# Kernel tuning notes

Hardware: AMD Instinct MI355X
Metric: run time of the kernel (lower is better)

## Reference

```python
import jax, jax.numpy as jnp
import numpy as np

B, K, D = 16384, 64, 256
H, HD = 2, 128  # n_heads, head_dim


def setup_inputs() -> dict:
    key = jax.random.key(0)
    ks = jax.random.split(key, 8)
    center_emb = jax.random.normal(ks[0], (B, D), dtype=jnp.float32)
    neighbor_emb = jax.random.normal(ks[1], (B, K, D), dtype=jnp.float32)
    neighbor_weights = jax.random.normal(ks[2], (B, K), dtype=jnp.float32)
    neighbor_mask = jax.random.randint(ks[3], (B, K), 0, 2).astype(bool)
    s = 1.0 / np.sqrt(D)
    Wq = jax.random.normal(ks[4], (H, HD, D), dtype=jnp.float32) * s   # per-head q proj
    Wk = jax.random.normal(ks[5], (H, HD, D), dtype=jnp.float32) * s   # per-head k proj
    Wout = jax.random.normal(ks[6], (D, H * D), dtype=jnp.float32) * (1.0 / np.sqrt(H * D))
    Wgate = jax.random.normal(ks[7], (D, 2 * D), dtype=jnp.float32) * (1.0 / np.sqrt(2 * D))
    return {"center_emb": center_emb, "neighbor_emb": neighbor_emb,
            "neighbor_weights": neighbor_weights, "neighbor_mask": neighbor_mask,
            "Wq": Wq, "Wk": Wk, "Wout": Wout, "Wgate": Wgate}


def reference(center_emb, neighbor_emb, neighbor_weights, neighbor_mask, Wq, Wk, Wout, Wgate):
    scale = 1.0 / jnp.sqrt(jnp.asarray(HD, dtype=center_emb.dtype))
    q = jnp.einsum('bd,hed->bhe', center_emb, Wq)          # [B,H,HD]
    k = jnp.einsum('bkd,hed->bhke', neighbor_emb, Wk)      # [B,H,K,HD]
    scores = jnp.einsum('bhe,bhke->bhk', q, k) * scale + neighbor_weights[:, None, :]
    scores = jnp.where(neighbor_mask[:, None, :], scores, jnp.asarray(-1e9, scores.dtype))
    attn = jax.nn.softmax(scores, axis=-1)                 # [B,H,K]
    ctx = jnp.einsum('bhk,bkd->bhd', attn, neighbor_emb)   # [B,H,D]
    multi_ctx = ctx.reshape(ctx.shape[0], H * D)           # concat heads along feature dim
    projected = multi_ctx @ Wout.T                         # [B,D]
    gate_in = jnp.concatenate([center_emb, projected], axis=-1)
    gate = jax.nn.sigmoid(gate_in @ Wgate.T)
    return gate * center_emb + (1.0 - gate) * projected
```

## Files before the change

kernel.cpp:

```cpp
#include <hip/hip_runtime.h>
#include <stdint.h>

typedef __attribute__((ext_vector_type(8))) short bf8;
typedef __attribute__((ext_vector_type(4))) float f4;

template<int CTRL>
__device__ __forceinline__ float dppMove(float v, float ident) {
  return __int_as_float(__builtin_amdgcn_update_dpp(
      __float_as_int(ident), __float_as_int(v), CTRL, 0xf, 0xf, false));
}
__device__ __forceinline__ float waveSum63(float v) {
  v += dppMove<0x128>(v, 0.f);
  v += dppMove<0x124>(v, 0.f);
  v += dppMove<0x122>(v, 0.f);
  v += dppMove<0x121>(v, 0.f);
  v += dppMove<0x142>(v, 0.f);
  v += dppMove<0x143>(v, 0.f);
  return v;
}
__device__ __forceinline__ float waveMax63(float v) {
  v = fmaxf(v, dppMove<0x128>(v, -3e38f));
  v = fmaxf(v, dppMove<0x124>(v, -3e38f));
  v = fmaxf(v, dppMove<0x122>(v, -3e38f));
  v = fmaxf(v, dppMove<0x121>(v, -3e38f));
  v = fmaxf(v, dppMove<0x142>(v, -3e38f));
  v = fmaxf(v, dppMove<0x143>(v, -3e38f));
  return v;
}
__device__ __forceinline__ float bcast63(float v) {
  return __int_as_float(__builtin_amdgcn_readlane(__float_as_int(v), 63));
}
__device__ __forceinline__ ushort f2bf(float f) {
  uint32_t b = __float_as_uint(f);
  uint32_t r = (b + 0x7fffu + ((b >> 16) & 1u)) >> 16;
  return (ushort)r;
}
__device__ __forceinline__ float bf2f(ushort u) {
  return __uint_as_float(((uint32_t)u) << 16);
}

__global__ __launch_bounds__(256)
void mhna_prologue(const float* __restrict__ center, ushort* __restrict__ centerBf,
                   const float* __restrict__ Wout, const float* __restrict__ Wgate,
                   ushort* __restrict__ Woutb, ushort* __restrict__ Wgb,
                   const float* __restrict__ Wq, const float* __restrict__ Wk,
                   ushort* __restrict__ Mtb) {
  const int blk = blockIdx.x;
  const int t = threadIdx.x;
  if (blk < 2048) {
    const int n4 = 16384 * 256 / 4;
    int i = blk * 256 + t;
    for (; i < n4; i += 2048 * 256) {
      float4 v = ((const float4*)center)[i];
      ushort4 u;
      u.x = f2bf(v.x); u.y = f2bf(v.y); u.z = f2bf(v.z); u.w = f2bf(v.w);
      ((ushort4*)centerBf)[i] = u;
    }
  } else if (blk < 2304) {
    const int n4 = 256 * 512 / 4;
    int i = (blk - 2048) * 256 + t;
    const float* s = (i < n4) ? Wout : Wgate;
    ushort* d = (i < n4) ? Woutb : Wgb;
    int j = (i < n4) ? i : i - n4;
    float4 v = ((const float4*)s)[j];
    ushort4 u;
    u.x = f2bf(v.x); u.y = f2bf(v.y); u.z = f2bf(v.z); u.w = f2bf(v.w);
    ((ushort4*)d)[j] = u;
  } else {
    const int n = blk - 2304;
    const int h = n >> 8, dk = n & 255;
    float acc = 0.f;
#pragma unroll 8
    for (int e = 0; e < 128; ++e) {
      float wkv = Wk[(size_t)(h * 128 + e) * 256 + dk];
      float wqv = Wq[(size_t)(h * 128 + e) * 256 + t];
      acc = fmaf(wqv, wkv, acc);
    }
    Mtb[(size_t)n * 256 + t] = f2bf(acc);
  }
}

__global__ __launch_bounds__(512)
void gemm_qM(const ushort* __restrict__ A, const ushort* __restrict__ W,
             ushort* __restrict__ Cb) {
  const int t = threadIdx.x;
  const int w = t >> 6, l = t & 63;
  const int row0 = blockIdx.x * 64;
  const int col0 = w * 64;
  const int lr = l & 15, lg = l >> 4;

  f4 acc[4][4];
#pragma unroll
  for (int i = 0; i < 4; ++i)
#pragma unroll
    for (int j = 0; j < 4; ++j) acc[i][j] = (f4)0.f;

#pragma unroll 2
  for (int kk = 0; kk < 256; kk += 32) {
    bf8 af[4];
#pragma unroll
    for (int i = 0; i < 4; ++i)
      af[i] = *(const bf8*)(A + (size_t)(row0 + i * 16 + lr) * 256 + kk + lg * 8);
#pragma unroll
    for (int j = 0; j < 4; ++j) {
      bf8 bw = *(const bf8*)(W + (size_t)(col0 + j * 16 + lr) * 256 + kk + lg * 8);
#pragma unroll
      for (int i = 0; i < 4; ++i)
        acc[i][j] = __builtin_amdgcn_mfma_f32_16x16x32_bf16(af[i], bw, acc[i][j], 0, 0, 0);
    }
  }
#pragma unroll
  for (int i = 0; i < 4; ++i)
#pragma unroll
    for (int j = 0; j < 4; ++j)
#pragma unroll
      for (int r = 0; r < 4; ++r)
        Cb[(size_t)(row0 + i * 16 + lg * 4 + r) * 512 + col0 + j * 16 + lr] =
            f2bf(acc[i][j][r]);
}

__global__ __launch_bounds__(256)
void mhna_kC(const float* __restrict__ nbg, const ushort* __restrict__ qMb,
             const float* __restrict__ wts, const int* __restrict__ msk,
             ushort* __restrict__ ctxb) {
  __shared__ float sc_s[2][64];
  __shared__ float at_s[2][64];
  __shared__ float part[4][512];
  const int b = blockIdx.x;
  const int t = threadIdx.x;
  const int w = t >> 6, lam = t & 63;

  const int mv_l = msk[(size_t)b * 64 + lam];
  const unsigned long long mb = __ballot(mv_l != 0);

  const ushort4* qm4 = (const ushort4*)(qMb + (size_t)b * 512);
  ushort4 ua = qm4[lam];
  ushort4 ub = qm4[64 + lam];
  f4 qa = {bf2f(ua.x), bf2f(ua.y), bf2f(ua.z), bf2f(ua.w)};
  f4 qb = {bf2f(ub.x), bf2f(ub.y), bf2f(ub.z), bf2f(ub.w)};

  const float4* nb4 = (const float4*)(nbg + (size_t)b * (64 * 256));
  float4 st[16];
#pragma unroll
  for (int r = 0; r < 16; ++r) {
    st[r] = make_float4(0.f, 0.f, 0.f, 0.f);
    const int k = r * 4 + w;
    if ((mb >> k) & 1ull) st[r] = nb4[k * 64 + lam];
  }

#pragma unroll
  for (int r = 0; r < 16; ++r) {
    const int k = r * 4 + w;
    if ((mb >> k) & 1ull) {
      float4 v = st[r];
      float p0 = v.x * qa.x + v.y * qa.y + v.z * qa.z + v.w * qa.w;
      float p1 = v.x * qb.x + v.y * qb.y + v.z * qb.z + v.w * qb.w;
      float s0 = waveSum63(p0);
      float s1 = waveSum63(p1);
      if (lam == 63) { sc_s[0][k] = s0; sc_s[1][k] = s1; }
    }
  }
  __syncthreads();

  if (t < 128) {
    const int h = w;
    float s = sc_s[h][lam];
    float wv = wts[(size_t)b * 64 + lam];
    s = mv_l ? fmaf(s, 0.08838834764831845f, wv) : -1e9f;
    float mx = bcast63(waveMax63(s));
    float e = __expf(s - mx);
    float sm = bcast63(waveSum63(e));
    at_s[h][lam] = e / sm;
  }
  __syncthreads();

  float c0[4] = {0.f, 0.f, 0.f, 0.f};
  float c1[4] = {0.f, 0.f, 0.f, 0.f};
#pragma unroll
  for (int r = 0; r < 16; ++r) {
    const int k = r * 4 + w;
    if ((mb >> k) & 1ull) {
      const float A0 = at_s[0][k];
      const float A1 = at_s[1][k];
      float4 v = st[r];
      c0[0] = fmaf(A0, v.x, c0[0]); c0[1] = fmaf(A0, v.y, c0[1]);
      c0[2] = fmaf(A0, v.z, c0[2]); c0[3] = fmaf(A0, v.w, c0[3]);
      c1[0] = fmaf(A1, v.x, c1[0]); c1[1] = fmaf(A1, v.y, c1[1]);
      c1[2] = fmaf(A1, v.z, c1[2]); c1[3] = fmaf(A1, v.w, c1[3]);
    }
  }
  f4 p0v = {c0[0], c0[1], c0[2], c0[3]};
  f4 p1v = {c1[0], c1[1], c1[2], c1[3]};
  *(f4*)&part[w][lam * 4]       = p0v;
  *(f4*)&part[w][256 + lam * 4] = p1v;
  __syncthreads();

  float r0 = part[0][t] + part[1][t] + part[2][t] + part[3][t];
  float r1 = part[0][256 + t] + part[1][256 + t] + part[2][256 + t] + part[3][256 + t];
  ctxb[(size_t)b * 512 + t] = f2bf(r0);
  ctxb[(size_t)b * 512 + 256 + t] = f2bf(r1);
}

#define LDP 260
__global__ __launch_bounds__(512)
void mhna_PG(const ushort* __restrict__ ctxb, const ushort* __restrict__ Woutb,
             const ushort* __restrict__ centerBf, const ushort* __restrict__ Wgb,
             const float* __restrict__ centerF, float* __restrict__ out) {
  __shared__ float p_s[64][LDP];
  const int t = threadIdx.x;
  const int w = t >> 6, l = t & 63;
  const int row0 = blockIdx.x * 64;
  const int col0 = w * 32;
  const int lr = l & 15, lg = l >> 4;

  f4 acc1[4][2];
#pragma unroll
  for (int i = 0; i < 4; ++i)
#pragma unroll
    for (int j = 0; j < 2; ++j) acc1[i][j] = (f4)0.f;

#pragma unroll 2
  for (int kk = 0; kk < 512; kk += 32) {
    bf8 af[4];
#pragma unroll
    for (int i = 0; i < 4; ++i)
      af[i] = *(const bf8*)(ctxb + (size_t)(row0 + i * 16 + lr) * 512 + kk + lg * 8);
#pragma unroll
    for (int j = 0; j < 2; ++j) {
      bf8 bw = *(const bf8*)(Woutb + (size_t)(col0 + j * 16 + lr) * 512 + kk + lg * 8);
#pragma unroll
      for (int i = 0; i < 4; ++i)
        acc1[i][j] = __builtin_amdgcn_mfma_f32_16x16x32_bf16(af[i], bw, acc1[i][j], 0, 0, 0);
    }
  }
#pragma unroll
  for (int i = 0; i < 4; ++i)
#pragma unroll
    for (int j = 0; j < 2; ++j)
#pragma unroll
      for (int r = 0; r < 4; ++r)
        p_s[i * 16 + lg * 4 + r][col0 + j * 16 + lr] = acc1[i][j][r];
  __syncthreads();

  f4 acc2[4][2];
#pragma unroll
  for (int i = 0; i < 4; ++i)
#pragma unroll
    for (int j = 0; j < 2; ++j) acc2[i][j] = (f4)0.f;

#pragma unroll 2
  for (int kk = 0; kk < 256; kk += 32) {
    bf8 af[4];
#pragma unroll
    for (int i = 0; i < 4; ++i)
      af[i] = *(const bf8*)(centerBf + (size_t)(row0 + i * 16 + lr) * 256 + kk + lg * 8);
#pragma unroll
    for (int j = 0; j < 2; ++j) {
      bf8 bw = *(const bf8*)(Wgb + (size_t)(col0 + j * 16 + lr) * 512 + kk + lg * 8);
#pragma unroll
      for (int i = 0; i < 4; ++i)
        acc2[i][j] = __builtin_amdgcn_mfma_f32_16x16x32_bf16(af[i], bw, acc2[i][j], 0, 0, 0);
    }
  }
#pragma unroll 2
  for (int kk = 0; kk < 256; kk += 32) {
    bf8 af[4];
#pragma unroll
    for (int i = 0; i < 4; ++i) {
      f4 x0 = *(const f4*)&p_s[i * 16 + lr][kk + lg * 8];
      f4 x1 = *(const f4*)&p_s[i * 16 + lr][kk + lg * 8 + 4];
      bf8 a;
      a[0] = (short)f2bf(x0.x); a[1] = (short)f2bf(x0.y);
      a[2] = (short)f2bf(x0.z); a[3] = (short)f2bf(x0.w);
      a[4] = (short)f2bf(x1.x); a[5] = (short)f2bf(x1.y);
      a[6] = (short)f2bf(x1.z); a[7] = (short)f2bf(x1.w);
      af[i] = a;
    }
#pragma unroll
    for (int j = 0; j < 2; ++j) {
      bf8 bw = *(const bf8*)(Wgb + (size_t)(col0 + j * 16 + lr) * 512 + 256 + kk + lg * 8);
#pragma unroll
      for (int i = 0; i < 4; ++i)
        acc2[i][j] = __builtin_amdgcn_mfma_f32_16x16x32_bf16(af[i], bw, acc2[i][j], 0, 0, 0);
    }
  }

#pragma unroll
  for (int i = 0; i < 4; ++i)
#pragma unroll
    for (int j = 0; j < 2; ++j)
#pragma unroll
      for (int r = 0; r < 4; ++r) {
        const int lrow = i * 16 + lg * 4 + r;
        const int row = row0 + lrow;
        const int col = col0 + j * 16 + lr;
        float g = 1.f / (1.f + __expf(-acc2[i][j][r]));
        float pv = p_s[lrow][col];
        float cv = centerF[(size_t)row * 256 + col];
        out[(size_t)row * 256 + col] = g * cv + (1.f - g) * pv;
      }
}

extern "C" void kernel_launch(void* const* d_in, const int* in_sizes, int n_in,
                              void* d_out, int out_size, void* d_ws, size_t ws_size,
                              hipStream_t stream) {
  const float* center = (const float*)d_in[0];
  const float* neigh  = (const float*)d_in[1];
  const float* nw     = (const float*)d_in[2];
  const int*   nm     = (const int*)d_in[3];
  const float* Wq     = (const float*)d_in[4];
  const float* Wk     = (const float*)d_in[5];
  const float* Wout   = (const float*)d_in[6];
  const float* Wgate  = (const float*)d_in[7];
  float* out = (float*)d_out;

  char* ws = (char*)d_ws;
  size_t off = 0;
  ushort* Mtb      = (ushort*)(ws + off); off += (size_t)512 * 256 * 2;
  ushort* centerBf = (ushort*)(ws + off); off += (size_t)16384 * 256 * 2;
  ushort* qMb      = (ushort*)(ws + off); off += (size_t)16384 * 512 * 2;
  ushort* ctxb     = (ushort*)(ws + off); off += (size_t)16384 * 512 * 2;
  ushort* Woutb    = (ushort*)(ws + off); off += (size_t)256 * 512 * 2;
  ushort* Wgb      = (ushort*)(ws + off); off += (size_t)256 * 512 * 2;

  mhna_prologue<<<2816, 256, 0, stream>>>(center, centerBf, Wout, Wgate,
                                          Woutb, Wgb, Wq, Wk, Mtb);
  gemm_qM<<<256, 512, 0, stream>>>(centerBf, Mtb, qMb);
  mhna_kC<<<16384, 256, 0, stream>>>(neigh, qMb, nw, nm, ctxb);
  mhna_PG<<<256, 512, 0, stream>>>(ctxb, Woutb, centerBf, Wgb, center, out);
}
```

Baseline: 198.8 us.

## Use MFMA for attention scores, stage neighbors as bf16 in LDS, halve GEMM tiles

The attention kernel now converts each neighbor row to bf16, computes both heads' scores with one MFMA per K-slice, and stores the bf16 rows in a swizzled LDS tile. The context sum then reads that tile per output column, which removes the cross-wave partial-sum buffer and the DPP reductions. The two GEMM kernels switch to 32-row tiles with twice as many blocks to raise occupancy. The final blend reads center from the bf16 copy instead of fp32, so accuracy drops slightly and the output now depends on bf16 center values.

Measured after the change: 295.0 us. 1.48x slower.

```diff
diff --git a/kernel.cpp b/kernel.cpp
--- a/kernel.cpp
+++ b/kernel.cpp
@@ -1,4 +1,5 @@
 #include <hip/hip_runtime.h>
+#include <hip/hip_bf16.h>
 #include <stdint.h>
 
 typedef __attribute__((ext_vector_type(8))) short bf8;
@@ -85,32 +86,32 @@
              ushort* __restrict__ Cb) {
   const int t = threadIdx.x;
   const int w = t >> 6, l = t & 63;
-  const int row0 = blockIdx.x * 64;
+  const int row0 = blockIdx.x * 32;
   const int col0 = w * 64;
   const int lr = l & 15, lg = l >> 4;
 
-  f4 acc[4][4];
-#pragma unroll
-  for (int i = 0; i < 4; ++i)
+  f4 acc[2][4];
+#pragma unroll
+  for (int i = 0; i < 2; ++i)
 #pragma unroll
     for (int j = 0; j < 4; ++j) acc[i][j] = (f4)0.f;
 
 #pragma unroll 2
   for (int kk = 0; kk < 256; kk += 32) {
-    bf8 af[4];
-#pragma unroll
-    for (int i = 0; i < 4; ++i)
+    bf8 af[2];
+#pragma unroll
+    for (int i = 0; i < 2; ++i)
       af[i] = *(const bf8*)(A + (size_t)(row0 + i * 16 + lr) * 256 + kk + lg * 8);
 #pragma unroll
     for (int j = 0; j < 4; ++j) {
       bf8 bw = *(const bf8*)(W + (size_t)(col0 + j * 16 + lr) * 256 + kk + lg * 8);
 #pragma unroll
-      for (int i = 0; i < 4; ++i)
+      for (int i = 0; i < 2; ++i)
         acc[i][j] = __builtin_amdgcn_mfma_f32_16x16x32_bf16(af[i], bw, acc[i][j], 0, 0, 0);
     }
   }
 #pragma unroll
-  for (int i = 0; i < 4; ++i)
+  for (int i = 0; i < 2; ++i)
 #pragma unroll
     for (int j = 0; j < 4; ++j)
 #pragma unroll
@@ -123,118 +124,125 @@
 void mhna_kC(const float* __restrict__ nbg, const ushort* __restrict__ qMb,
              const float* __restrict__ wts, const int* __restrict__ msk,
              ushort* __restrict__ ctxb) {
+  __shared__ ushort nb_s[64][256];
   __shared__ float sc_s[2][64];
   __shared__ float at_s[2][64];
-  __shared__ float part[4][512];
   const int b = blockIdx.x;
   const int t = threadIdx.x;
-  const int w = t >> 6, lam = t & 63;
-
-  const int mv_l = msk[(size_t)b * 64 + lam];
+  const int w = t >> 6, l = t & 63;
+  const int lr = l & 15, lg = l >> 4;
+  const int krow = w * 16 + lr;
+
+  const int mv_l = msk[(size_t)b * 64 + l];
   const unsigned long long mb = __ballot(mv_l != 0);
-
-  const ushort4* qm4 = (const ushort4*)(qMb + (size_t)b * 512);
-  ushort4 ua = qm4[lam];
-  ushort4 ub = qm4[64 + lam];
-  f4 qa = {bf2f(ua.x), bf2f(ua.y), bf2f(ua.z), bf2f(ua.w)};
-  f4 qb = {bf2f(ub.x), bf2f(ub.y), bf2f(ub.z), bf2f(ub.w)};
-
-  const float4* nb4 = (const float4*)(nbg + (size_t)b * (64 * 256));
-  float4 st[16];
-#pragma unroll
-  for (int r = 0; r < 16; ++r) {
-    st[r] = make_float4(0.f, 0.f, 0.f, 0.f);
-    const int k = r * 4 + w;
-    if ((mb >> k) & 1ull) st[r] = nb4[k * 64 + lam];
-  }
-
-#pragma unroll
-  for (int r = 0; r < 16; ++r) {
-    const int k = r * 4 + w;
-    if ((mb >> k) & 1ull) {
-      float4 v = st[r];
-      float p0 = v.x * qa.x + v.y * qa.y + v.z * qa.z + v.w * qa.w;
-      float p1 = v.x * qb.x + v.y * qb.y + v.z * qb.z + v.w * qb.w;
-      float s0 = waveSum63(p0);
-      float s1 = waveSum63(p1);
-      if (lam == 63) { sc_s[0][k] = s0; sc_s[1][k] = s1; }
-    }
+  const bool rowOn = (mb >> krow) & 1ull;
+
+  const float* nbrow = nbg + (size_t)b * 16384 + (size_t)krow * 256 + lg * 8;
+  float4 a0[8], a1[8];
+#pragma unroll
+  for (int s = 0; s < 8; ++s) {
+    if (rowOn) {
+      a0[s] = *(const float4*)(nbrow + s * 32);
+      a1[s] = *(const float4*)(nbrow + s * 32 + 4);
+    } else {
+      a0[s] = make_float4(0.f, 0.f, 0.f, 0.f);
+      a1[s] = make_float4(0.f, 0.f, 0.f, 0.f);
+    }
+  }
+  bf8 bwv[8];
+#pragma unroll
+  for (int s = 0; s < 8; ++s) {
+    if (lr < 2)
+      bwv[s] = *(const bf8*)(qMb + (size_t)b * 512 + lr * 256 + s * 32 + lg * 8);
+    else
+      bwv[s] = (bf8)0;
+  }
+
+  f4 acc = {0.f, 0.f, 0.f, 0.f};
+  const int swz = (krow & 7) << 4;
+  char* ldsrow = (char*)&nb_s[krow][0];
+#pragma unroll
+  for (int s = 0; s < 8; ++s) {
+    __hip_bfloat162 c0 = __float22bfloat162_rn(make_float2(a0[s].x, a0[s].y));
+    __hip_bfloat162 c1 = __float22bfloat162_rn(make_float2(a0[s].z, a0[s].w));
+    __hip_bfloat162 c2 = __float22bfloat162_rn(make_float2(a1[s].x, a1[s].y));
+    __hip_bfloat162 c3 = __float22bfloat162_rn(make_float2(a1[s].z, a1[s].w));
+    union { bf8 v; uint32_t u[4]; } cv;
+    cv.u[0] = *reinterpret_cast<uint32_t*>(&c0);
+    cv.u[1] = *reinterpret_cast<uint32_t*>(&c1);
+    cv.u[2] = *reinterpret_cast<uint32_t*>(&c2);
+    cv.u[3] = *reinterpret_cast<uint32_t*>(&c3);
+    acc = __builtin_amdgcn_mfma_f32_16x16x32_bf16(cv.v, bwv[s], acc, 0, 0, 0);
+    *(uint4*)(ldsrow + ((s * 64 + lg * 16) ^ swz)) = *(uint4*)&cv.u[0];
+  }
+  if (lr < 2) {
+#pragma unroll
+    for (int r = 0; r < 4; ++r)
+      sc_s[lr][w * 16 + lg * 4 + r] = acc[r];
   }
   __syncthreads();
 
   if (t < 128) {
     const int h = w;
-    float s = sc_s[h][lam];
-    float wv = wts[(size_t)b * 64 + lam];
+    float s = sc_s[h][l];
+    float wv = wts[(size_t)b * 64 + l];
     s = mv_l ? fmaf(s, 0.08838834764831845f, wv) : -1e9f;
     float mx = bcast63(waveMax63(s));
     float e = __expf(s - mx);
     float sm = bcast63(waveSum63(e));
-    at_s[h][lam] = e / sm;
+    at_s[h][l] = e / sm;
   }
   __syncthreads();
 
-  float c0[4] = {0.f, 0.f, 0.f, 0.f};
-  float c1[4] = {0.f, 0.f, 0.f, 0.f};
-#pragma unroll
-  for (int r = 0; r < 16; ++r) {
-    const int k = r * 4 + w;
-    if ((mb >> k) & 1ull) {
-      const float A0 = at_s[0][k];
-      const float A1 = at_s[1][k];
-      float4 v = st[r];
-      c0[0] = fmaf(A0, v.x, c0[0]); c0[1] = fmaf(A0, v.y, c0[1]);
-      c0[2] = fmaf(A0, v.z, c0[2]); c0[3] = fmaf(A0, v.w, c0[3]);
-      c1[0] = fmaf(A1, v.x, c1[0]); c1[1] = fmaf(A1, v.y, c1[1]);
-      c1[2] = fmaf(A1, v.z, c1[2]); c1[3] = fmaf(A1, v.w, c1[3]);
-    }
-  }
-  f4 p0v = {c0[0], c0[1], c0[2], c0[3]};
-  f4 p1v = {c1[0], c1[1], c1[2], c1[3]};
-  *(f4*)&part[w][lam * 4]       = p0v;
-  *(f4*)&part[w][256 + lam * 4] = p1v;
-  __syncthreads();
-
-  float r0 = part[0][t] + part[1][t] + part[2][t] + part[3][t];
-  float r1 = part[0][256 + t] + part[1][256 + t] + part[2][256 + t] + part[3][256 + t];
-  ctxb[(size_t)b * 512 + t] = f2bf(r0);
-  ctxb[(size_t)b * 512 + 256 + t] = f2bf(r1);
+  float acc0 = 0.f, acc1 = 0.f;
+  const char* ldsbase = (const char*)&nb_s[0][0];
+#pragma unroll 4
+  for (int k = 0; k < 64; ++k) {
+    if (!((mb >> k) & 1ull)) continue;
+    const ushort us = *(const ushort*)(ldsbase + (size_t)k * 512 +
+                                       ((2 * t) ^ ((k & 7) << 4)));
+    float v = bf2f(us);
+    acc0 = fmaf(at_s[0][k], v, acc0);
+    acc1 = fmaf(at_s[1][k], v, acc1);
+  }
+  ctxb[(size_t)b * 512 + t] = f2bf(acc0);
+  ctxb[(size_t)b * 512 + 256 + t] = f2bf(acc1);
 }
 
 #define LDP 260
 __global__ __launch_bounds__(512)
 void mhna_PG(const ushort* __restrict__ ctxb, const ushort* __restrict__ Woutb,
              const ushort* __restrict__ centerBf, const ushort* __restrict__ Wgb,
-             const float* __restrict__ centerF, float* __restrict__ out) {
-  __shared__ float p_s[64][LDP];
+             float* __restrict__ out) {
+  __shared__ float p_s[32][LDP];
   const int t = threadIdx.x;
   const int w = t >> 6, l = t & 63;
-  const int row0 = blockIdx.x * 64;
+  const int row0 = blockIdx.x * 32;
   const int col0 = w * 32;
   const int lr = l & 15, lg = l >> 4;
 
-  f4 acc1[4][2];
-#pragma unroll
-  for (int i = 0; i < 4; ++i)
+  f4 acc1[2][2];
+#pragma unroll
+  for (int i = 0; i < 2; ++i)
 #pragma unroll
     for (int j = 0; j < 2; ++j) acc1[i][j] = (f4)0.f;
 
 #pragma unroll 2
   for (int kk = 0; kk < 512; kk += 32) {
-    bf8 af[4];
-#pragma unroll
-    for (int i = 0; i < 4; ++i)
+    bf8 af[2];
+#pragma unroll
+    for (int i = 0; i < 2; ++i)
       af[i] = *(const bf8*)(ctxb + (size_t)(row0 + i * 16 + lr) * 512 + kk + lg * 8);
 #pragma unroll
     for (int j = 0; j < 2; ++j) {
       bf8 bw = *(const bf8*)(Woutb + (size_t)(col0 + j * 16 + lr) * 512 + kk + lg * 8);
 #pragma unroll
-      for (int i = 0; i < 4; ++i)
+      for (int i = 0; i < 2; ++i)
         acc1[i][j] = __builtin_amdgcn_mfma_f32_16x16x32_bf16(af[i], bw, acc1[i][j], 0, 0, 0);
     }
   }
 #pragma unroll
-  for (int i = 0; i < 4; ++i)
+  for (int i = 0; i < 2; ++i)
 #pragma unroll
     for (int j = 0; j < 2; ++j)
 #pragma unroll
@@ -242,51 +250,55 @@
         p_s[i * 16 + lg * 4 + r][col0 + j * 16 + lr] = acc1[i][j][r];
   __syncthreads();
 
-  f4 acc2[4][2];
-#pragma unroll
-  for (int i = 0; i < 4; ++i)
+  f4 acc2[2][2];
+#pragma unroll
+  for (int i = 0; i < 2; ++i)
 #pragma unroll
     for (int j = 0; j < 2; ++j) acc2[i][j] = (f4)0.f;
 
 #pragma unroll 2
   for (int kk = 0; kk < 256; kk += 32) {
-    bf8 af[4];
-#pragma unroll
-    for (int i = 0; i < 4; ++i)
+    bf8 af[2];
+#pragma unroll
+    for (int i = 0; i < 2; ++i)
       af[i] = *(const bf8*)(centerBf + (size_t)(row0 + i * 16 + lr) * 256 + kk + lg * 8);
 #pragma unroll
     for (int j = 0; j < 2; ++j) {
       bf8 bw = *(const bf8*)(Wgb + (size_t)(col0 + j * 16 + lr) * 512 + kk + lg * 8);
 #pragma unroll
-      for (int i = 0; i < 4; ++i)
+      for (int i = 0; i < 2; ++i)
         acc2[i][j] = __builtin_amdgcn_mfma_f32_16x16x32_bf16(af[i], bw, acc2[i][j], 0, 0, 0);
     }
   }
 #pragma unroll 2
   for (int kk = 0; kk < 256; kk += 32) {
-    bf8 af[4];
-#pragma unroll
-    for (int i = 0; i < 4; ++i) {
+    bf8 af[2];
+#pragma unroll
+    for (int i = 0; i < 2; ++i) {
       f4 x0 = *(const f4*)&p_s[i * 16 + lr][kk + lg * 8];
       f4 x1 = *(const f4*)&p_s[i * 16 + lr][kk + lg * 8 + 4];
-      bf8 a;
-      a[0] = (short)f2bf(x0.x); a[1] = (short)f2bf(x0.y);
-      a[2] = (short)f2bf(x0.z); a[3] = (short)f2bf(x0.w);
-      a[4] = (short)f2bf(x1.x); a[5] = (short)f2bf(x1.y);
-      a[6] = (short)f2bf(x1.z); a[7] = (short)f2bf(x1.w);
-      af[i] = a;
+      __hip_bfloat162 c0 = __float22bfloat162_rn(make_float2(x0.x, x0.y));
+      __hip_bfloat162 c1 = __float22bfloat162_rn(make_float2(x0.z, x0.w));
+      __hip_bfloat162 c2 = __float22bfloat162_rn(make_float2(x1.x, x1.y));
+      __hip_bfloat162 c3 = __float22bfloat162_rn(make_float2(x1.z, x1.w));
+      union { bf8 v; uint32_t u[4]; } cv;
+      cv.u[0] = *reinterpret_cast<uint32_t*>(&c0);
+      cv.u[1] = *reinterpret_cast<uint32_t*>(&c1);
+      cv.u[2] = *reinterpret_cast<uint32_t*>(&c2);
+      cv.u[3] = *reinterpret_cast<uint32_t*>(&c3);
+      af[i] = cv.v;
     }
 #pragma unroll
     for (int j = 0; j < 2; ++j) {
       bf8 bw = *(const bf8*)(Wgb + (size_t)(col0 + j * 16 + lr) * 512 + 256 + kk + lg * 8);
 #pragma unroll
-      for (int i = 0; i < 4; ++i)
+      for (int i = 0; i < 2; ++i)
         acc2[i][j] = __builtin_amdgcn_mfma_f32_16x16x32_bf16(af[i], bw, acc2[i][j], 0, 0, 0);
     }
   }
 
 #pragma unroll
-  for (int i = 0; i < 4; ++i)
+  for (int i = 0; i < 2; ++i)
 #pragma unroll
     for (int j = 0; j < 2; ++j)
 #pragma unroll
@@ -296,7 +308,7 @@
         const int col = col0 + j * 16 + lr;
         float g = 1.f / (1.f + __expf(-acc2[i][j][r]));
         float pv = p_s[lrow][col];
-        float cv = centerF[(size_t)row * 256 + col];
+        float cv = bf2f(centerBf[(size_t)row * 256 + col]);
         out[(size_t)row * 256 + col] = g * cv + (1.f - g) * pv;
       }
 }
@@ -325,7 +337,7 @@
 
   mhna_prologue<<<2816, 256, 0, stream>>>(center, centerBf, Wout, Wgate,
                                           Woutb, Wgb, Wq, Wk, Mtb);
-  gemm_qM<<<256, 512, 0, stream>>>(centerBf, Mtb, qMb);
+  gemm_qM<<<512, 512, 0, stream>>>(centerBf, Mtb, qMb);
   mhna_kC<<<16384, 256, 0, stream>>>(neigh, qMb, nw, nm, ctxb);
-  mhna_PG<<<256, 512, 0, stream>>>(ctxb, Woutb, centerBf, Wgb, center, out);
-}
+  mhna_PG<<<512, 512, 0, stream>>>(ctxb, Woutb, centerBf, Wgb, out);
+}
```
